# Kernel tuning notes

Measured on AMD Instinct MI355X. Metric: run time of the kernel, lower is better.

The kernel has to match this reference:

```python
import jax, jax.numpy as jnp
import numpy as np
import math

B, S, D, H = 16, 1024, 768, 12
Dh = D // H  # 64


def setup_inputs() -> dict:
    key = jax.random.key(0)
    ks = jax.random.split(key, 9)
    scale = 1.0 / math.sqrt(D)
    X = jax.random.normal(ks[0], (B, S, D), dtype=jnp.float32)
    # Per-head Q/K/V projections stacked along head dim: [H, D, Dh]
    Wq = jax.random.normal(ks[1], (H, D, Dh), dtype=jnp.float32) * scale
    Wk = jax.random.normal(ks[2], (H, D, Dh), dtype=jnp.float32) * scale
    Wv = jax.random.normal(ks[3], (H, D, Dh), dtype=jnp.float32) * scale
    bq = jax.random.normal(ks[4], (H, Dh), dtype=jnp.float32) * scale
    bk = jax.random.normal(ks[5], (H, Dh), dtype=jnp.float32) * scale
    bv = jax.random.normal(ks[6], (H, Dh), dtype=jnp.float32) * scale
    Wo = jax.random.normal(ks[7], (D, D), dtype=jnp.float32) * scale
    bo = jax.random.normal(ks[8], (D,), dtype=jnp.float32) * scale
    return {"X": X, "Wq": Wq, "bq": bq, "Wk": Wk, "bk": bk,
            "Wv": Wv, "bv": bv, "Wo": Wo, "bo": bo}


def reference(X, Wq, bq, Wk, bk, Wv, bv, Wo, bo):
    # Batched multi-head QKV projections (equivalent to the per-head Linear loop).
    Q = jnp.einsum('bsd,hde->bhse', X, Wq) + bq[None, :, None, :]
    K = jnp.einsum('bsd,hde->bhse', X, Wk) + bk[None, :, None, :]
    V = jnp.einsum('bsd,hde->bhse', X, Wv) + bv[None, :, None, :]
    scores = jnp.einsum('bhse,bhte->bhst', Q, K) / jnp.sqrt(jnp.float32(Dh))
    A = jax.nn.softmax(scores, axis=-1)            # [B,H,S,S]
    O = jnp.einsum('bhst,bhte->bhse', A, V)        # [B,H,S,Dh]
    # Concat heads along feature dim (matches torch cat order: head 0 first).
    msa = jnp.transpose(O, (0, 2, 1, 3)).reshape(B, S, D)
    return msa @ Wo + bo
```

## Files before the change

### kernel.cpp

```cpp
#include <hip/hip_runtime.h>
#include <hip/hip_bf16.h>

#define BB 16
#define SS 1024
#define DD 768
#define HH 12
#define DH 64

typedef short short8 __attribute__((ext_vector_type(8)));
typedef float f32x4 __attribute__((ext_vector_type(4)));
typedef float f32x16 __attribute__((ext_vector_type(16)));
typedef unsigned int uv2 __attribute__((ext_vector_type(2)));

__device__ inline float b2f(unsigned short v) {
    union { unsigned int u; float f; } x; x.u = ((unsigned int)v) << 16; return x.f;
}
__device__ inline unsigned short f2b(float f) {
    unsigned int u = __float_as_uint(f);
    u += 0x7FFFu + ((u >> 16) & 1u);
    return (unsigned short)(u >> 16);
}
__device__ inline unsigned int pk2(float a, float b) {
    __hip_bfloat162 h = __float22bfloat162_rn(make_float2(a, b));
    return *(unsigned int*)&h;
}
__device__ __forceinline__ float fast_exp2(float x) {
#if __has_builtin(__builtin_amdgcn_exp2f)
    return __builtin_amdgcn_exp2f(x);
#else
    return exp2f(x);
#endif
}
__device__ inline void cvt8(unsigned short* dst, const float* src) {
    const float4 f0 = *(const float4*)src;
    const float4 f1 = *(const float4*)(src + 4);
    unsigned short t[8] = {f2b(f0.x), f2b(f0.y), f2b(f0.z), f2b(f0.w),
                           f2b(f1.x), f2b(f1.y), f2b(f1.z), f2b(f1.w)};
    *(uint4*)dst = *(const uint4*)t;
}
__device__ __forceinline__ void async16(const void* g, void* l) {
    __builtin_amdgcn_global_load_lds(
        (const __attribute__((address_space(1))) void*)g,
        (__attribute__((address_space(3))) void*)l, 16, 0, 0);
}

__global__ __launch_bounds__(256) void detect_kernel(const unsigned short* __restrict__ X,
                                                     int* __restrict__ flag) {
    __shared__ int s;
    if (threadIdx.x == 0) s = 0;
    __syncthreads();
    int c = 0;
    for (int i = threadIdx.x; i < 16384; i += 256) {
        unsigned short v = X[i];
        if ((v & 0x7FFFu) >= 0x7F80u) c = 1;
    }
    if (c) s = 1;
    __syncthreads();
    if (threadIdx.x == 0) flag[0] = s;
}

__global__ __launch_bounds__(256) void prep_all(
    const void* __restrict__ Xv,
    const void* __restrict__ Wqv, const void* __restrict__ bqv,
    const void* __restrict__ Wkv, const void* __restrict__ bkv,
    const void* __restrict__ Wvv, const void* __restrict__ bvv,
    const void* __restrict__ Wov, const void* __restrict__ bov,
    const int* __restrict__ flag,
    unsigned short* __restrict__ Xb, unsigned short* __restrict__ Wc,
    unsigned short* __restrict__ Wot, unsigned short* __restrict__ bc,
    float* __restrict__ bo32)
{
    __shared__ unsigned short Ls[64][72];
    const int dt = *flag;
    const int u = threadIdx.x;
    const int bx = blockIdx.x;

    if (bx < 6144) {
        size_t base = ((size_t)bx * 256 + u) * 8;
        if (dt) cvt8(Xb + base, (const float*)Xv + base);
        else    *(uint4*)(Xb + base) = *(const uint4*)((const unsigned short*)Xv + base);
        return;
    }
    if (bx < 6720) {
        const int idx = bx - 6144;
        const int kt = idx % 12;
        const int y  = idx / 12;
        const int rk = u >> 2;
        const int e0 = (u & 3) * 16;

        const void* src; size_t srcBase;
        unsigned short* dst; int drow;
        if (y < 36) {
            int z = y / 12, h = y % 12;
            src = (z == 0) ? Wqv : (z == 1) ? Wkv : Wvv;
            srcBase = ((size_t)h * DD + kt * 64 + rk) * DH;
            dst = Wc; drow = z * 768 + h * 64;
        } else {
            int nt = y - 36;
            src = Wov;
            srcBase = (size_t)(kt * 64 + rk) * DD + nt * 64;
            dst = Wot; drow = nt * 64;
        }
#pragma unroll
        for (int ii = 0; ii < 2; ++ii) {
            int e = e0 + ii * 8;
            if (dt) {
                const float* p = (const float*)src + srcBase + e;
                float4 a = *(const float4*)p, b = *(const float4*)(p + 4);
                float v[8] = {a.x, a.y, a.z, a.w, b.x, b.y, b.z, b.w};
#pragma unroll
                for (int j = 0; j < 8; ++j) Ls[e + j][rk] = f2b(v[j]);
            } else {
                union { uint4 v; unsigned short s[8]; } t;
                t.v = *(const uint4*)((const unsigned short*)src + srcBase + e);
#pragma unroll
                for (int j = 0; j < 8; ++j) Ls[e + j][rk] = t.s[j];
            }
        }
        __syncthreads();
        const int e = u >> 2, q = u & 3;
#pragma unroll
        for (int ii = 0; ii < 2; ++ii) {
            int kk = q * 16 + ii * 8;
            *(uint4*)(dst + (size_t)(drow + e) * DD + kt * 64 + kk) = *(const uint4*)(&Ls[e][kk]);
        }
        return;
    }
    for (int n = u; n < 2304; n += 256) {
        int z = n / 768, i = n % 768;
        const void* b = (z == 0) ? bqv : (z == 1) ? bkv : bvv;
        bc[n] = dt ? f2b(((const float*)b)[i]) : ((const unsigned short*)b)[i];
    }
    for (int n = u; n < 768; n += 256)
        bo32[n] = dt ? ((const float*)bov)[n] : b2f(((const unsigned short*)bov)[n]);
}

__global__ __launch_bounds__(256) void qkv_gemm(
    const unsigned short* __restrict__ Xb,
    const unsigned short* __restrict__ Wc,
    const unsigned short* __restrict__ bc,
    unsigned short* __restrict__ Qb, unsigned short* __restrict__ Kb,
    unsigned short* __restrict__ Vtb)
{
    __shared__ __align__(16) unsigned short lds[17408];
    unsigned short* As = lds;
    unsigned short* Bs = lds + 128 * 64;

    const int u = threadIdx.x;
    const int lane = u & 63, w = u >> 6;
    const int ln = lane & 15, quad = lane >> 4;
    const int wm = w & 1, wn = w >> 1;

    const int nt0 = blockIdx.x;
    const int m0  = blockIdx.y << 7;
    const int n0  = nt0 << 7;
    const int z   = nt0 / 6;
    const int hpair = (nt0 % 6) * 2;

    const int rA = w * 32 + (lane >> 3);
    const int c8 = (((lane & 7) ^ (lane >> 3)) * 8);

    f32x4 acc[4][4];
#pragma unroll
    for (int i = 0; i < 4; ++i)
#pragma unroll
        for (int j = 0; j < 4; ++j) acc[i][j] = (f32x4){0.f, 0.f, 0.f, 0.f};

    const unsigned short* Ag = Xb + (size_t)(m0 + rA) * DD + c8;
    const unsigned short* Bg = Wc + (size_t)(n0 + rA) * DD + c8;
    unsigned short* lA0 = As + w * 2048;
    unsigned short* lB0 = Bs + w * 2048;

    for (int kb = 0; kb < 12; ++kb) {
        const int k0 = kb * 64;
        if (kb) __syncthreads();
#pragma unroll
        for (int j = 0; j < 4; ++j) {
            async16(Ag + (size_t)j * 8 * DD + k0, lA0 + j * 512);
            async16(Bg + (size_t)j * 8 * DD + k0, lB0 + j * 512);
        }
        __syncthreads();
#pragma unroll
        for (int kh = 0; kh < 2; ++kh) {
            const int sx = ((kh * 4 + quad) ^ (ln & 7)) * 8;
            short8 af[4], bf[4];
#pragma unroll
            for (int t = 0; t < 4; ++t) {
                af[t] = *(const short8*)(As + (wm * 64 + t * 16 + ln) * 64 + sx);
                bf[t] = *(const short8*)(Bs + (wn * 64 + t * 16 + ln) * 64 + sx);
            }
#pragma unroll
            for (int mt = 0; mt < 4; ++mt)
#pragma unroll
                for (int nt = 0; nt < 4; ++nt)
                    acc[mt][nt] = __builtin_amdgcn_mfma_f32_16x16x32_bf16(af[mt], bf[nt], acc[mt][nt], 0, 0, 0);
        }
    }

    float bias[4];
#pragma unroll
    for (int nt = 0; nt < 4; ++nt) bias[nt] = b2f(bc[n0 + wn * 64 + nt * 16 + ln]);

    const int b = m0 >> 10;
    if (z < 2) {
        unsigned short* O = (z == 0) ? Qb : Kb;
        const float sc = (z == 0) ? 0.180336880111120f : 1.0f;
        const int h = hpair + wn;
        const int sb = (m0 & 1023) + wm * 64;
#pragma unroll
        for (int mt = 0; mt < 4; ++mt)
#pragma unroll
            for (int r = 0; r < 4; ++r) {
                int s = sb + mt * 16 + quad * 4 + r;
                size_t rowo = ((size_t)(b * HH + h) * SS + s) * DH;
#pragma unroll
                for (int nt = 0; nt < 4; ++nt)
                    O[rowo + nt * 16 + ln] = f2b((acc[mt][nt][r] + bias[nt]) * sc);
            }
    } else {
        __syncthreads();
#pragma unroll
        for (int mt = 0; mt < 4; ++mt)
#pragma unroll
            for (int nt = 0; nt < 4; ++nt)
#pragma unroll
                for (int r = 0; r < 4; ++r)
                    lds[(wn * 64 + nt * 16 + ln) * 136 + wm * 64 + mt * 16 + quad * 4 + r] =
                        f2b(acc[mt][nt][r] + bias[nt]);
        __syncthreads();
        const int cc = u >> 1, half = u & 1;
        const int h = hpair + (cc >> 6), e = cc & 63;
        const int sb = (m0 & 1023) + half * 64;
        unsigned short* dst = Vtb + ((size_t)(b * HH + h) * DH + e) * SS + sb;
        const unsigned short* srcp = lds + cc * 136 + half * 64;
#pragma unroll
        for (int i = 0; i < 8; ++i)
            *(uint4*)(dst + i * 8) = *(const uint4*)(srcp + i * 8);
    }
}

__global__ __launch_bounds__(256, 4) void attn_kernel(
    const unsigned short* __restrict__ Kb,
    const unsigned short* __restrict__ Vtb,
    unsigned short* __restrict__ Qb)
{
    __shared__ __align__(16) unsigned short Ks[2][4096];
    __shared__ __align__(16) unsigned short Vs[2][4096];
    unsigned short* KsF = &Ks[0][0];

    const int u = threadIdx.x;
    const int flat = (blockIdx.y << 3) | blockIdx.x;
    const int swz  = (flat & 7) * 192 + (flat >> 3);
    const int s0 = (swz & 7) << 7;
    const int bh = swz >> 3;

    const int lane = u & 63, w = u >> 6;
    const int l31 = lane & 31, hi = lane >> 5;
    const int r7 = l31 & 7;

    unsigned short* Qg = Qb + ((size_t)bh * SS + s0) * DH;
    const unsigned short* Kg = Kb + (size_t)bh * SS * DH;
    const unsigned short* Vg = Vtb + (size_t)bh * DH * SS;

    const int srow = lane >> 3;
    const int cg8  = ((lane & 7) ^ srow) * 8;

    const unsigned short* kp0 = Kg + (size_t)((w * 2 + 0) * 8 + srow) * DH + cg8;
    const unsigned short* kp1 = Kg + (size_t)((w * 2 + 1) * 8 + srow) * DH + cg8;
    const unsigned short* vp0 = Vg + (size_t)((w * 2 + 0) * 8 + srow) * SS + cg8;
    const unsigned short* vp1 = Vg + (size_t)((w * 2 + 1) * 8 + srow) * SS + cg8;

#pragma unroll
    for (int j = 0; j < 4; ++j) {
        const int r0 = (w * 4 + j) * 8 + srow;
        async16(Qg + (size_t)r0 * DH + cg8, KsF + (w * 4 + j) * 512);
    }
    __syncthreads();

    short8 qf[4];
    {
        const unsigned short* qrow = KsF + (w * 32 + l31) * 64;
#pragma unroll
        for (int ke = 0; ke < 4; ++ke)
            qf[ke] = *(const short8*)(qrow + (((ke * 2 + hi) ^ r7) * 8));
    }
    __syncthreads();

    async16(kp0, &Ks[0][(w * 2 + 0) * 512]);
    async16(kp1, &Ks[0][(w * 2 + 1) * 512]);
    async16(vp0, &Vs[0][(w * 2 + 0) * 512]);
    async16(vp1, &Vs[0][(w * 2 + 1) * 512]);
    kp0 += 64 * DH; kp1 += 64 * DH; vp0 += 64; vp1 += 64;
    __syncthreads();

    short8 ones;
#pragma unroll
    for (int i = 0; i < 8; ++i) ones[i] = (short)0x3F80;

    int off[4];
#pragma unroll
    for (int x = 0; x < 4; ++x) off[x] = l31 * 64 + (((x * 2 + hi) ^ r7) * 8);

    f32x16 oA, oB, oL;
#pragma unroll
    for (int i = 0; i < 16; ++i) { oA[i] = 0.f; oB[i] = 0.f; oL[i] = 0.f; }

    for (int kt = 0; kt < 16; ++kt) {
        const int cur = kt & 1;
        if (kt < 15) {
            unsigned short* lk = &Ks[cur ^ 1][(w * 2) * 512];
            unsigned short* lv = &Vs[cur ^ 1][(w * 2) * 512];
            async16(kp0, lk);
            async16(kp1, lk + 512);
            async16(vp0, lv);
            async16(vp1, lv + 512);
            kp0 += 64 * DH; kp1 += 64 * DH; vp0 += 64; vp1 += 64;
        }
        const unsigned short* kc = Ks[cur];
        const unsigned short* vc = Vs[cur];

        f32x16 sA, sB;
#pragma unroll
        for (int i = 0; i < 16; ++i) { sA[i] = 0.f; sB[i] = 0.f; }
        __builtin_amdgcn_s_setprio(1);
#pragma unroll
        for (int ke = 0; ke < 4; ++ke) {
            short8 kf0 = *(const short8*)(kc + off[ke]);
            short8 kf1 = *(const short8*)(kc + off[ke] + 2048);
            sA = __builtin_amdgcn_mfma_f32_32x32x16_bf16(kf0, qf[ke], sA, 0, 0, 0);
            sB = __builtin_amdgcn_mfma_f32_32x32x16_bf16(kf1, qf[ke], sB, 0, 0, 0);
        }
        __builtin_amdgcn_s_setprio(0);

        unsigned int W0[8], W1[8];
#pragma unroll
        for (int i = 0; i < 8; ++i) {
            W0[i] = pk2(fast_exp2(sA[2 * i]), fast_exp2(sA[2 * i + 1]));
            W1[i] = pk2(fast_exp2(sB[2 * i]), fast_exp2(sB[2 * i + 1]));
        }

        __builtin_amdgcn_s_setprio(1);
#define PV_STEP(Wt, ks) {                                                              \
        union { unsigned int wv[4]; short8 s; } pu;                                    \
        { uv2 rr = __builtin_amdgcn_permlane32_swap(Wt[4 * ((ks) & 1) + 0],            \
                                                    Wt[4 * ((ks) & 1) + 2], false, false); \
          pu.wv[0] = rr.x; pu.wv[2] = rr.y; }                                          \
        { uv2 rr = __builtin_amdgcn_permlane32_swap(Wt[4 * ((ks) & 1) + 1],            \
                                                    Wt[4 * ((ks) & 1) + 3], false, false); \
          pu.wv[1] = rr.x; pu.wv[3] = rr.y; }                                          \
        oL = __builtin_amdgcn_mfma_f32_32x32x16_bf16(ones, pu.s, oL, 0, 0, 0);         \
        short8 vf0 = *(const short8*)(vc + off[(ks)]);                                 \
        short8 vf1 = *(const short8*)(vc + off[(ks)] + 2048);                          \
        oA = __builtin_amdgcn_mfma_f32_32x32x16_bf16(vf0, pu.s, oA, 0, 0, 0);          \
        oB = __builtin_amdgcn_mfma_f32_32x32x16_bf16(vf1, pu.s, oB, 0, 0, 0); }
        PV_STEP(W0, 0)
        PV_STEP(W0, 1)
        PV_STEP(W1, 2)
        PV_STEP(W1, 3)
#undef PV_STEP
        __builtin_amdgcn_s_setprio(0);

        __syncthreads();
    }

    const float linv = 1.f / oL[0];

    unsigned short* Ob = KsF + w * 2048;
#define OSTORE(oc, et) {                                                   \
        _Pragma("unroll")                                                  \
        for (int rg = 0; rg < 4; ++rg) {                                   \
            uv2 wv;                                                        \
            wv.x = pk2(oc[rg * 4 + 0] * linv, oc[rg * 4 + 1] * linv);      \
            wv.y = pk2(oc[rg * 4 + 2] * linv, oc[rg * 4 + 3] * linv);      \
            *(uv2*)(Ob + l31 * 64 + ((((et) * 4 + rg) ^ r7) * 8) + hi * 4) = wv; \
        } }
    OSTORE(oA, 0)
    OSTORE(oB, 1)
#undef OSTORE

    const int rr2 = lane >> 1, q16 = lane & 1, rs = rr2 & 7;
    const unsigned short* orow = KsF + w * 2048 + rr2 * 64;
    unsigned short* gout = Qg + (size_t)(w * 32 + rr2) * DH;
#pragma unroll
    for (int i = 0; i < 4; ++i) {
        const int g = q16 * 4 + i;
        *(uint4*)(gout + g * 8) = *(const uint4*)(orow + ((g ^ rs) * 8));
    }
}

__global__ __launch_bounds__(256) void oproj_gemm(
    const unsigned short* __restrict__ Ob,
    const unsigned short* __restrict__ Wot,
    const float* __restrict__ bo32,
    float* __restrict__ out)
{
    __shared__ __align__(16) unsigned short lds[128 * 128];
    unsigned short* As = lds;
    unsigned short* Bs = lds + 128 * 64;

    const int u = threadIdx.x;
    const int lane = u & 63, w = u >> 6;
    const int ln = lane & 15, quad = lane >> 4;
    const int wm = w & 1, wn = w >> 1;

    const int n0 = blockIdx.x << 7;
    const int m0 = blockIdx.y << 7;
    const int b = m0 >> 10, s0t = m0 & 1023;

    const int rA = w * 32 + (lane >> 3);
    const int c8 = (((lane & 7) ^ (lane >> 3)) * 8);

    f32x4 acc[4][4];
#pragma unroll
    for (int i = 0; i < 4; ++i)
#pragma unroll
        for (int j = 0; j < 4; ++j) acc[i][j] = (f32x4){0.f, 0.f, 0.f, 0.f};

    const unsigned short* Bg = Wot + (size_t)(n0 + rA) * DD + c8;
    unsigned short* lA0 = As + w * 2048;
    unsigned short* lB0 = Bs + w * 2048;

    for (int kb = 0; kb < 12; ++kb) {
        if (kb) __syncthreads();
        const unsigned short* Ag = Ob + ((size_t)(b * HH + kb) * SS + s0t + rA) * DH + c8;
#pragma unroll
        for (int j = 0; j < 4; ++j) {
            async16(Ag + (size_t)j * 8 * DH, lA0 + j * 512);
            async16(Bg + (size_t)j * 8 * DD + kb * 64, lB0 + j * 512);
        }
        __syncthreads();
#pragma unroll
        for (int kh = 0; kh < 2; ++kh) {
            const int sx = ((kh * 4 + quad) ^ (ln & 7)) * 8;
            short8 af[4], bf[4];
#pragma unroll
            for (int t = 0; t < 4; ++t) {
                af[t] = *(const short8*)(As + (wm * 64 + t * 16 + ln) * 64 + sx);
                bf[t] = *(const short8*)(Bs + (wn * 64 + t * 16 + ln) * 64 + sx);
            }
#pragma unroll
            for (int mt = 0; mt < 4; ++mt)
#pragma unroll
                for (int nt = 0; nt < 4; ++nt)
                    acc[mt][nt] = __builtin_amdgcn_mfma_f32_16x16x32_bf16(af[mt], bf[nt], acc[mt][nt], 0, 0, 0);
        }
    }

    float bias[4];
#pragma unroll
    for (int nt = 0; nt < 4; ++nt) bias[nt] = bo32[n0 + wn * 64 + nt * 16 + ln];
#pragma unroll
    for (int mt = 0; mt < 4; ++mt)
#pragma unroll
        for (int r = 0; r < 4; ++r) {
            int m = m0 + wm * 64 + mt * 16 + quad * 4 + r;
            float* orow = out + (size_t)m * DD + n0 + wn * 64;
#pragma unroll
            for (int nt = 0; nt < 4; ++nt)
                orow[nt * 16 + ln] = acc[mt][nt][r] + bias[nt];
        }
}

extern "C" void kernel_launch(void* const* d_in, const int* in_sizes, int n_in,
                              void* d_out, int out_size, void* d_ws, size_t ws_size,
                              hipStream_t stream)
{
    const void* X  = d_in[0];
    const void* Wq = d_in[1];
    const void* bq = d_in[2];
    const void* Wk = d_in[3];
    const void* bk = d_in[4];
    const void* Wv = d_in[5];
    const void* bv = d_in[6];
    const void* Wo = d_in[7];
    const void* bo = d_in[8];
    float* out = (float*)d_out;

    const size_t NE = (size_t)BB * HH * SS * DH;
    char* p = (char*)d_ws;
    int* flag = (int*)p;                 p += 256;
    unsigned short* Qb  = (unsigned short*)p;  p += NE * 2;
    unsigned short* Kb  = (unsigned short*)p;  p += NE * 2;
    unsigned short* Vtb = (unsigned short*)p;  p += NE * 2;
    unsigned short* Xb  = (unsigned short*)p;  p += (size_t)BB * SS * DD * 2;
    unsigned short* Wc  = (unsigned short*)p;  p += (size_t)3 * DD * DD * 2;
    unsigned short* Wot = (unsigned short*)p;  p += (size_t)DD * DD * 2;
    unsigned short* bcb = (unsigned short*)p;  p += 4608;
    float* bo32 = (float*)p;                   p += 3072;

    detect_kernel<<<1, 256, 0, stream>>>((const unsigned short*)X, flag);
    prep_all<<<6721, 256, 0, stream>>>(X, Wq, bq, Wk, bk, Wv, bv, Wo, bo, flag,
                                       Xb, Wc, Wot, bcb, bo32);
    qkv_gemm<<<dim3(18, 128), 256, 0, stream>>>(Xb, Wc, bcb, Qb, Kb, Vtb);
    attn_kernel<<<dim3(8, 192), 256, 0, stream>>>(Kb, Vtb, Qb);
    oproj_gemm<<<dim3(6, 128), 256, 0, stream>>>(Qb, Wot, bo32, out);
}
```

Before: 288.6 us.

## Double-buffer LDS in projection GEMMs and remap blocks for XCD locality

Both the QKV and output-projection GEMMs now prefetch the next K-slice into a second LDS buffer while the MFMAs run on the current one. This replaces the two barriers per iteration with one at the end of each step. The block index is also remapped so that consecutive tiles land on the same XCD, which is meant to improve L2 reuse of the X and weight tiles. In exchange, LDS use per block grows to 64 KB, which may cut how many blocks fit on a CU.

```diff
diff --git a/kernel.cpp b/kernel.cpp
--- a/kernel.cpp
+++ b/kernel.cpp
@@ -142,19 +142,19 @@
     unsigned short* __restrict__ Qb, unsigned short* __restrict__ Kb,
     unsigned short* __restrict__ Vtb)
 {
-    __shared__ __align__(16) unsigned short lds[17408];
-    unsigned short* As = lds;
-    unsigned short* Bs = lds + 128 * 64;
+    __shared__ __align__(16) unsigned short lds[32768];
 
     const int u = threadIdx.x;
     const int lane = u & 63, w = u >> 6;
     const int ln = lane & 15, quad = lane >> 4;
     const int wm = w & 1, wn = w >> 1;
 
-    const int nt0 = blockIdx.x;
-    const int m0  = blockIdx.y << 7;
-    const int n0  = nt0 << 7;
-    const int z   = nt0 / 6;
+    const int flat = blockIdx.y * 18 + blockIdx.x;
+    const int sf   = (flat & 7) * 288 + (flat >> 3);
+    const int nt0  = sf % 18;
+    const int m0   = (sf / 18) << 7;
+    const int n0   = nt0 << 7;
+    const int z    = nt0 / 6;
     const int hpair = (nt0 % 6) * 2;
 
     const int rA = w * 32 + (lane >> 3);
@@ -168,18 +168,32 @@
 
     const unsigned short* Ag = Xb + (size_t)(m0 + rA) * DD + c8;
     const unsigned short* Bg = Wc + (size_t)(n0 + rA) * DD + c8;
-    unsigned short* lA0 = As + w * 2048;
-    unsigned short* lB0 = Bs + w * 2048;
+
+    {
+        unsigned short* lA = lds + w * 2048;
+        unsigned short* lB = lds + 8192 + w * 2048;
+#pragma unroll
+        for (int j = 0; j < 4; ++j) {
+            async16(Ag + (size_t)j * 8 * DD, lA + j * 512);
+            async16(Bg + (size_t)j * 8 * DD, lB + j * 512);
+        }
+    }
+    __syncthreads();
 
     for (int kb = 0; kb < 12; ++kb) {
-        const int k0 = kb * 64;
-        if (kb) __syncthreads();
-#pragma unroll
-        for (int j = 0; j < 4; ++j) {
-            async16(Ag + (size_t)j * 8 * DD + k0, lA0 + j * 512);
-            async16(Bg + (size_t)j * 8 * DD + k0, lB0 + j * 512);
-        }
-        __syncthreads();
+        const int cur = kb & 1;
+        if (kb < 11) {
+            unsigned short* lA = lds + (cur ^ 1) * 16384 + w * 2048;
+            unsigned short* lB = lds + (cur ^ 1) * 16384 + 8192 + w * 2048;
+            const int k0 = (kb + 1) * 64;
+#pragma unroll
+            for (int j = 0; j < 4; ++j) {
+                async16(Ag + (size_t)j * 8 * DD + k0, lA + j * 512);
+                async16(Bg + (size_t)j * 8 * DD + k0, lB + j * 512);
+            }
+        }
+        const unsigned short* As = lds + cur * 16384;
+        const unsigned short* Bs = As + 8192;
 #pragma unroll
         for (int kh = 0; kh < 2; ++kh) {
             const int sx = ((kh * 4 + quad) ^ (ln & 7)) * 8;
@@ -195,6 +209,7 @@
                 for (int nt = 0; nt < 4; ++nt)
                     acc[mt][nt] = __builtin_amdgcn_mfma_f32_16x16x32_bf16(af[mt], bf[nt], acc[mt][nt], 0, 0, 0);
         }
+        __syncthreads();
     }
 
     float bias[4];
@@ -394,17 +409,17 @@
     const float* __restrict__ bo32,
     float* __restrict__ out)
 {
-    __shared__ __align__(16) unsigned short lds[128 * 128];
-    unsigned short* As = lds;
-    unsigned short* Bs = lds + 128 * 64;
+    __shared__ __align__(16) unsigned short lds[32768];
 
     const int u = threadIdx.x;
     const int lane = u & 63, w = u >> 6;
     const int ln = lane & 15, quad = lane >> 4;
     const int wm = w & 1, wn = w >> 1;
 
-    const int n0 = blockIdx.x << 7;
-    const int m0 = blockIdx.y << 7;
+    const int flat = blockIdx.y * 6 + blockIdx.x;
+    const int sf   = (flat & 7) * 96 + (flat >> 3);
+    const int n0   = (sf % 6) << 7;
+    const int m0   = (sf / 6) << 7;
     const int b = m0 >> 10, s0t = m0 & 1023;
 
     const int rA = w * 32 + (lane >> 3);
@@ -417,18 +432,33 @@
         for (int j = 0; j < 4; ++j) acc[i][j] = (f32x4){0.f, 0.f, 0.f, 0.f};
 
     const unsigned short* Bg = Wot + (size_t)(n0 + rA) * DD + c8;
-    unsigned short* lA0 = As + w * 2048;
-    unsigned short* lB0 = Bs + w * 2048;
+
+    {
+        unsigned short* lA = lds + w * 2048;
+        unsigned short* lB = lds + 8192 + w * 2048;
+        const unsigned short* Agk = Ob + ((size_t)(b * HH + 0) * SS + s0t + rA) * DH + c8;
+#pragma unroll
+        for (int j = 0; j < 4; ++j) {
+            async16(Agk + (size_t)j * 8 * DH, lA + j * 512);
+            async16(Bg + (size_t)j * 8 * DD, lB + j * 512);
+        }
+    }
+    __syncthreads();
 
     for (int kb = 0; kb < 12; ++kb) {
-        if (kb) __syncthreads();
-        const unsigned short* Ag = Ob + ((size_t)(b * HH + kb) * SS + s0t + rA) * DH + c8;
-#pragma unroll
-        for (int j = 0; j < 4; ++j) {
-            async16(Ag + (size_t)j * 8 * DH, lA0 + j * 512);
-            async16(Bg + (size_t)j * 8 * DD + kb * 64, lB0 + j * 512);
-        }
-        __syncthreads();
+        const int cur = kb & 1;
+        if (kb < 11) {
+            unsigned short* lA = lds + (cur ^ 1) * 16384 + w * 2048;
+            unsigned short* lB = lds + (cur ^ 1) * 16384 + 8192 + w * 2048;
+            const unsigned short* Agk = Ob + ((size_t)(b * HH + kb + 1) * SS + s0t + rA) * DH + c8;
+#pragma unroll
+            for (int j = 0; j < 4; ++j) {
+                async16(Agk + (size_t)j * 8 * DH, lA + j * 512);
+                async16(Bg + (size_t)j * 8 * DD + (kb + 1) * 64, lB + j * 512);
+            }
+        }
+        const unsigned short* As = lds + cur * 16384;
+        const unsigned short* Bs = As + 8192;
 #pragma unroll
         for (int kh = 0; kh < 2; ++kh) {
             const int sx = ((kh * 4 + quad) ^ (ln & 7)) * 8;
@@ -444,6 +474,7 @@
                 for (int nt = 0; nt < 4; ++nt)
                     acc[mt][nt] = __builtin_amdgcn_mfma_f32_16x16x32_bf16(af[mt], bf[nt], acc[mt][nt], 0, 0, 0);
         }
+        __syncthreads();
     }
 
     float bias[4];
```

Result: slower. 299.1 us (+3.6%).
